# Kernel tuning notes

Hardware: AMD Instinct MI355X
Metric: run time of the kernel (lower is better)

The kernel has to match this reference:

```python
import jax, jax.numpy as jnp
import numpy as np

B, N, D, K, L, H, DFF = 2048, 64, 256, 32, 2, 8, 1024
TEMP = 10.0
EPS = 1e-10


def _ln(x, g, b):
    m = jnp.mean(x, -1, keepdims=True)
    v = jnp.mean((x - m) ** 2, -1, keepdims=True)
    return (x - m) * jax.lax.rsqrt(v + 1e-5) * g + b


def _mha(x, Wqkv, bqkv, Wo, bo):
    b, n, d = x.shape
    dh = d // H
    qkv = x @ Wqkv.T + bqkv                      # [b,n,3d]
    q, k, v = jnp.split(qkv, 3, axis=-1)
    q = q.reshape(b, n, H, dh)
    k = k.reshape(b, n, H, dh)
    v = v.reshape(b, n, H, dh)
    att = jnp.einsum('bqhd,bkhd->bhqk', q, k) / np.float32(np.sqrt(dh))
    att = jax.nn.softmax(att, axis=-1)
    o = jnp.einsum('bhqk,bkhd->bqhd', att, v).reshape(b, n, d)
    return o @ Wo.T + bo


def _encoder(x, Wqkv, bqkv, Wo, bo, ln1_g, ln1_b, ln2_g, ln2_b, W1, b1, W2, b2):
    # torch TransformerEncoder, norm_first=False (post-LN), dropout=0
    for l in range(L):
        x = _ln(x + _mha(x, Wqkv[l], bqkv[l], Wo[l], bo[l]), ln1_g[l], ln1_b[l])
        h = jax.nn.relu(x @ W1[l].T + b1[l]) @ W2[l].T + b2[l]
        x = _ln(x + h, ln2_g[l], ln2_b[l])
    return x


def _cluster_probs_from_emb(emb, mus):
    # ||x - tanh(mu)||^2 via expansion to avoid the [B,N,K,D] intermediate
    mt = jnp.tanh(mus)                                       # [K,D]
    d2 = (jnp.sum(emb ** 2, -1)[..., None]
          - 2.0 * jnp.einsum('bnd,kd->bnk', emb, mt)
          + jnp.sum(mt ** 2, -1))                            # [B,N,K]
    e = jnp.exp(-d2 / TEMP)
    return e / jnp.sum(e, -1, keepdims=True)


def _forward(input_series, init_logits, transition_logits,
             Wqkv, bqkv, Wo, bo, ln1_g, ln1_b, ln2_g, ln2_b,
             W1, b1, W2, b2, mus):
    prob_pi = jax.nn.softmax(init_logits, axis=0)            # [K]
    prob_A = jax.nn.softmax(transition_logits, axis=1)       # [K,K]
    emb_all = _encoder(input_series, Wqkv, bqkv, Wo, bo,
                       ln1_g, ln1_b, ln2_g, ln2_b, W1, b1, W2, b2)
    logits_all = _cluster_probs_from_emb(emb_all, mus)       # [B,N,K]

    log_emit = jnp.log(logits_all + EPS)                     # [B,N,K]
    lt0 = jax.nn.softmax(jnp.log(prob_pi + EPS)[None, :] + log_emit[:, 0], axis=1)

    def step(lt, le):
        lt = jax.nn.softmax(jnp.log(lt @ prob_A + EPS) + le, axis=1)
        return lt, lt

    _, rest = jax.lax.scan(step, lt0, jnp.swapaxes(log_emit[:, 1:], 0, 1))
    cluster_probs = jnp.concatenate([lt0[:, None], jnp.swapaxes(rest, 0, 1)], axis=1)
    entropy_loss = -jnp.mean(jnp.sum(cluster_probs * jnp.log(cluster_probs + EPS), -1))
    return cluster_probs, emb_all, prob_pi, prob_A, entropy_loss


def setup_inputs() -> dict:
    key = jax.random.key(0)
    ks = jax.random.split(key, 10)
    s = jnp.float32(0.02)
    return {
        'input_series': jax.random.normal(ks[0], (B, N, D), jnp.float32),
        'init_logits': jax.random.normal(ks[1], (K,), jnp.float32),
        'transition_logits': jax.random.normal(ks[2], (K, K), jnp.float32),
        'Wqkv': jax.random.normal(ks[3], (L, 3 * D, D), jnp.float32) * s,
        'bqkv': jnp.zeros((L, 3 * D), jnp.float32),
        'Wo': jax.random.normal(ks[4], (L, D, D), jnp.float32) * s,
        'bo': jnp.zeros((L, D), jnp.float32),
        'ln1_g': jnp.ones((L, D), jnp.float32),
        'ln1_b': jnp.zeros((L, D), jnp.float32),
        'ln2_g': jnp.ones((L, D), jnp.float32),
        'ln2_b': jnp.zeros((L, D), jnp.float32),
        'W1': jax.random.normal(ks[5], (L, DFF, D), jnp.float32) * s,
        'b1': jnp.zeros((L, DFF), jnp.float32),
        'W2': jax.random.normal(ks[6], (L, D, DFF), jnp.float32) * s,
        'b2': jnp.zeros((L, D), jnp.float32),
        'mus': jax.random.normal(ks[7], (K, D), jnp.float32),
    }


def reference(input_series, init_logits, transition_logits, Wqkv, bqkv, Wo, bo,
              ln1_g, ln1_b, ln2_g, ln2_b, W1, b1, W2, b2, mus):
    return _forward(input_series, init_logits, transition_logits, Wqkv, bqkv,
                    Wo, bo, ln1_g, ln1_b, ln2_g, ln2_b, W1, b1, W2, b2, mus)
```

## Files before the change

### kernel.cpp

```cpp
#include <hip/hip_runtime.h>

#define BB   2048
#define NNX  64
#define DD   256
#define KKC  32
#define LLN  2
#define HHN  8
#define DHH  32
#define DFFN 1024
#define BNT  (BB*NNX)

typedef short s16x8 __attribute__((ext_vector_type(8)));
typedef float f32x4 __attribute__((ext_vector_type(4)));

#define GLOAD_LDS16(gp, lp) __builtin_amdgcn_global_load_lds( \
    (const __attribute__((address_space(1))) void*)(gp),      \
    (__attribute__((address_space(3))) void*)(lp), 16, 0, 0)

#define WAITVM4() asm volatile("s_waitcnt vmcnt(4)" ::: "memory")
#define WAITVM0() asm volatile("s_waitcnt vmcnt(0)" ::: "memory")
#define WAITLGKM0() do { asm volatile("s_waitcnt lgkmcnt(0)" ::: "memory"); \
                         __builtin_amdgcn_sched_barrier(0); } while (0)
#define SBAR() __builtin_amdgcn_s_barrier()

__device__ __forceinline__ unsigned short f2bf(float f) {
  unsigned int u = __float_as_uint(f);
  u += 0x7fffu + ((u >> 16) & 1u);
  return (unsigned short)(u >> 16);
}
__device__ __forceinline__ float bf2f(unsigned short u) {
  return __uint_as_float(((unsigned int)u) << 16);
}

__device__ __forceinline__ unsigned char f2fp8(float f) {
  unsigned u = __float_as_uint(f);
  unsigned lsb = (u >> 20) & 1u;
  u += 0x7FFFFu + lsb;
  int e = (int)((u >> 23) & 255u) - 120;
  if (e <= 0) {
    int q = (int)(f * 512.f + 0.5f);
    return (unsigned char)q;
  }
  if (e > 15) return 0x7E;
  return (unsigned char)((e << 3) | ((u >> 20) & 7u));
}
__device__ __forceinline__ unsigned char f2fp8s(float f) {
  unsigned s = __float_as_uint(f) >> 31;
  float a = fminf(fabsf(f), 448.f);
  return (unsigned char)((s << 7) | f2fp8(a));
}

__global__ __launch_bounds__(256) void cvt_kernel(const float4* __restrict__ src,
                                                  ushort4* __restrict__ dst, int n4) {
  int i = blockIdx.x * 256 + threadIdx.x;
  int st = gridDim.x * 256;
  for (; i < n4; i += st) {
    float4 v = src[i];
    ushort4 o;
    o.x = f2bf(v.x); o.y = f2bf(v.y); o.z = f2bf(v.z); o.w = f2bf(v.w);
    dst[i] = o;
  }
}

__global__ __launch_bounds__(256) void cvtw_kernel(const float4* __restrict__ wq, ushort4* __restrict__ dq,
                                                   const float4* __restrict__ wo, ushort4* __restrict__ dov,
                                                   const float4* __restrict__ w1, ushort4* __restrict__ d1,
                                                   const float4* __restrict__ w2, uchar4* __restrict__ d2) {
  const int n0 = 98304, n1 = 32768, n2 = 131072, n3 = 131072;
  int i = blockIdx.x * 256 + threadIdx.x;
  int st = gridDim.x * 256;
  for (; i < n0 + n1 + n2 + n3; i += st) {
    int j = i;
    if (j < n0) {
      float4 v = wq[j];
      dq[j] = (ushort4){f2bf(v.x), f2bf(v.y), f2bf(v.z), f2bf(v.w)};
    } else if ((j -= n0) < n1) {
      float4 v = wo[j];
      dov[j] = (ushort4){f2bf(v.x), f2bf(v.y), f2bf(v.z), f2bf(v.w)};
    } else if ((j -= n1) < n2) {
      float4 v = w1[j];
      d1[j] = (ushort4){f2bf(v.x), f2bf(v.y), f2bf(v.z), f2bf(v.w)};
    } else {
      j -= n2;
      float4 v = w2[j];
      d2[j] = (uchar4){f2fp8s(v.x * 64.f), f2fp8s(v.y * 64.f),
                       f2fp8s(v.z * 64.f), f2fp8s(v.w * 64.f)};
    }
  }
}

__global__ void mt_kernel(const float* __restrict__ mus, unsigned short* __restrict__ mtb,
                          float* __restrict__ mtn) {
  int k = threadIdx.x;
  if (k < 32) {
    float acc = 0.f;
    for (int d = 0; d < 256; d++) {
      float t = tanhf(mus[k * 256 + d]);
      mtb[k * 264 + d] = f2bf(t);
      acc += t * t;
    }
    mtn[k] = acc;
  }
}

__global__ void piA_kernel(const float* __restrict__ il, const float* __restrict__ tl,
                           float* __restrict__ d_pi, float* __restrict__ d_A,
                           float* __restrict__ d_ent) {
  int lane = threadIdx.x;
  if (lane == 0) *d_ent = 0.f;
  if (lane < 32) {
    float v = il[lane];
    float mx = v;
    #pragma unroll
    for (int off = 16; off; off >>= 1) mx = fmaxf(mx, __shfl_xor(mx, off, 32));
    float e = expf(v - mx), sm = e;
    #pragma unroll
    for (int off = 16; off; off >>= 1) sm += __shfl_xor(sm, off, 32);
    d_pi[lane] = e / sm;
    for (int r = 0; r < 32; r++) {
      float a = tl[r * 32 + lane];
      float m2 = a;
      #pragma unroll
      for (int off = 16; off; off >>= 1) m2 = fmaxf(m2, __shfl_xor(m2, off, 32));
      float e2 = expf(a - m2), s2 = e2;
      #pragma unroll
      for (int off = 16; off; off >>= 1) s2 += __shfl_xor(s2, off, 32);
      d_A[r * 32 + lane] = e2 / s2;
    }
  }
}

template <int EPI>
__global__ __launch_bounds__(256, 4) void gemm_nt(const unsigned short* __restrict__ A,
                                                  const unsigned short* __restrict__ Bw,
                                                  const float* __restrict__ bias,
                                                  void* __restrict__ outp,
                                                  int N, int K, int nx) {
  __shared__ unsigned short lds[16384];
  const int t = threadIdx.x;
  const int bid = blockIdx.x, nwg = gridDim.x;
  const int wg = (bid & 7) * (nwg >> 3) + (bid >> 3);
  const int m0 = (wg / nx) << 7;
  const int n0 = (wg % nx) << 7;
  const int lane = t & 63, w = t >> 6;
  const int wm = w >> 1, wn = w & 1;
  const int lr = lane & 15, lk = lane >> 4;

  const int r0 = t >> 2, sg = t & 3;
  const int s0 = sg ^ ((r0 >> 1) & 3);
  const int r1 = r0 + 64;
  const int s1 = sg ^ ((r1 >> 1) & 3);
  const int aoff0 = (m0 + r0) * K + s0 * 8;
  const int aoff1 = (m0 + r1) * K + s1 * 8;
  const int boff0 = (n0 + r0) * K + s0 * 8;
  const int boff1 = (n0 + r1) * K + s1 * 8;

#define STAGE(buf, k0) do {                                    \
    char* la = (char*)lds + (buf) * 16384;                     \
    GLOAD_LDS16(A + aoff0 + (k0), la + t * 16);                \
    GLOAD_LDS16(A + aoff1 + (k0), la + 4096 + t * 16);         \
    GLOAD_LDS16(Bw + boff0 + (k0), la + 8192 + t * 16);        \
    GLOAD_LDS16(Bw + boff1 + (k0), la + 12288 + t * 16);       \
  } while (0)

  f32x4 acc[4][4];
  #pragma unroll
  for (int i = 0; i < 4; i++)
    #pragma unroll
    for (int j = 0; j < 4; j++) acc[i][j] = (f32x4)(0.f);

  const int ra = wm * 64 + lr, rb = wn * 64 + lr;
  const int sla = lk ^ ((ra >> 1) & 3), slb = lk ^ ((rb >> 1) & 3);

  const int NT = K >> 5;
  STAGE(0, 0);
  STAGE(1, 32);
  WAITVM4();
  SBAR();

  int c = 0;
  for (int kt = 0; kt < NT; kt++) {
    s16x8 af[4], bf[4];
    {
      const unsigned short* ua = lds + c * 8192;
      const unsigned short* ub = ua + 4096;
      #pragma unroll
      for (int mf = 0; mf < 4; mf++)
        af[mf] = *(const s16x8*)&ua[(ra + mf * 16) * 32 + sla * 8];
      #pragma unroll
      for (int nf = 0; nf < 4; nf++)
        bf[nf] = *(const s16x8*)&ub[(rb + nf * 16) * 32 + slb * 8];
    }
    __builtin_amdgcn_s_setprio(1);
    #pragma unroll
    for (int mf = 0; mf < 4; mf++)
      #pragma unroll
      for (int nf = 0; nf < 4; nf++)
        acc[mf][nf] = __builtin_amdgcn_mfma_f32_16x16x32_bf16(af[mf], bf[nf], acc[mf][nf], 0, 0, 0);
    __builtin_amdgcn_s_setprio(0);
    SBAR();
    if (kt < NT - 2) {
      STAGE(c, (kt + 2) << 5);
      WAITVM4();
    } else if (kt == NT - 2) {
      WAITVM0();
    }
    SBAR();
    c ^= 1;
  }
#undef STAGE

  #pragma unroll
  for (int nf = 0; nf < 4; nf++) {
    int col = n0 + wn * 64 + nf * 16 + lr;
    float bv = bias[col];
    #pragma unroll
    for (int mf = 0; mf < 4; mf++)
      #pragma unroll
      for (int r = 0; r < 4; r++) {
        int row = m0 + wm * 64 + mf * 16 + lk * 4 + r;
        size_t o = (size_t)row * N + col;
        float v = acc[mf][nf][r] + bv;
        if (EPI == 0) {
          ((unsigned short*)outp)[o] = f2bf(v);
        } else {
          float h = fminf(fmaxf(v, 0.f) * 8.f, 448.f);
          ((unsigned char*)outp)[o] = f2fp8(h);
        }
      }
  }
}

template <bool WR32>
__global__ __launch_bounds__(512) void gemm_ln(const unsigned short* __restrict__ A,
                                               const unsigned short* __restrict__ Bw,
                                               const float* __restrict__ bias,
                                               const unsigned short* __restrict__ res,
                                               const float* __restrict__ g,
                                               const float* __restrict__ bta,
                                               unsigned short* __restrict__ xb,
                                               float* __restrict__ x32,
                                               int K) {
  __shared__ unsigned short As[128 * 64];
  __shared__ unsigned short Bs[256 * 64];
  __shared__ float stats[2][128][4];
  const int t = threadIdx.x;
  const int nwg = gridDim.x;
  const int bid = blockIdx.x;
  const int wg = (bid & 7) * (nwg >> 3) + (bid >> 3);
  const int m0 = wg << 7;

  const int lane = t & 63, w = t >> 6;
  const int wm = w >> 2, wn = w & 3;
  const int lr = lane & 15, lk = lane >> 4;

  size_t aoff[2], boff[4];
  #pragma unroll
  for (int p = 0; p < 2; p++) {
    int u = p * 512 + t;
    int row = u >> 3, sp = u & 7;
    int seg = sp ^ (((row >> 2) & 1) << 1);
    aoff[p] = (size_t)(m0 + row) * K + seg * 8;
  }
  #pragma unroll
  for (int p = 0; p < 4; p++) {
    int u = p * 512 + t;
    int row = u >> 3, sp = u & 7;
    int seg = sp ^ (((row >> 2) & 1) << 1);
    boff[p] = (size_t)row * K + seg * 8;
  }

  f32x4 acc[4][4];
  #pragma unroll
  for (int i = 0; i < 4; i++)
    #pragma unroll
    for (int j = 0; j < 4; j++) acc[i][j] = (f32x4)(0.f);

  for (int k0 = 0; k0 < K; k0 += 64) {
    #pragma unroll
    for (int p = 0; p < 2; p++)
      GLOAD_LDS16(A + aoff[p] + k0, (char*)As + (p * 512 + t) * 16);
    #pragma unroll
    for (int p = 0; p < 4; p++)
      GLOAD_LDS16(Bw + boff[p] + k0, (char*)Bs + (p * 512 + t) * 16);
    __syncthreads();
    #pragma unroll
    for (int z = 0; z < 2; z++) {
      s16x8 af[4], bfr[4];
      #pragma unroll
      for (int mf = 0; mf < 4; mf++) {
        int row = wm * 64 + mf * 16 + lr;
        int cc = (z * 4 + lk) ^ (((row >> 2) & 1) << 1);
        af[mf] = *(const s16x8*)&As[row * 64 + cc * 8];
      }
      #pragma unroll
      for (int nf = 0; nf < 4; nf++) {
        int row = wn * 64 + nf * 16 + lr;
        int cc = (z * 4 + lk) ^ (((row >> 2) & 1) << 1);
        bfr[nf] = *(const s16x8*)&Bs[row * 64 + cc * 8];
      }
      #pragma unroll
      for (int mf = 0; mf < 4; mf++)
        #pragma unroll
        for (int nf = 0; nf < 4; nf++)
          acc[mf][nf] = __builtin_amdgcn_mfma_f32_16x16x32_bf16(af[mf], bfr[nf], acc[mf][nf], 0, 0, 0);
    }
    __syncthreads();
  }

  float bv[4];
  #pragma unroll
  for (int nf = 0; nf < 4; nf++) bv[nf] = bias[wn * 64 + nf * 16 + lr];

  #pragma unroll
  for (int mf = 0; mf < 4; mf++) {
    #pragma unroll
    for (int r = 0; r < 4; r++) {
      int grow = m0 + wm * 64 + mf * 16 + lk * 4 + r;
      float s = 0.f, q = 0.f;
      #pragma unroll
      for (int nf = 0; nf < 4; nf++) {
        int col = wn * 64 + nf * 16 + lr;
        float v = acc[mf][nf][r] + bv[nf] + bf2f(res[(size_t)grow * 256 + col]);
        acc[mf][nf][r] = v;
        s += v; q += v * v;
      }
      #pragma unroll
      for (int off = 1; off < 16; off <<= 1) { s += __shfl_xor(s, off); q += __shfl_xor(q, off); }
      if (lr == 0) {
        int lrow = wm * 64 + mf * 16 + lk * 4 + r;
        stats[0][lrow][wn] = s;
        stats[1][lrow][wn] = q;
      }
    }
  }
  __syncthreads();

  float gv[4], bbv[4];
  #pragma unroll
  for (int nf = 0; nf < 4; nf++) {
    int col = wn * 64 + nf * 16 + lr;
    gv[nf] = g[col]; bbv[nf] = bta[col];
  }
  #pragma unroll
  for (int mf = 0; mf < 4; mf++) {
    #pragma unroll
    for (int r = 0; r < 4; r++) {
      int lrow = wm * 64 + mf * 16 + lk * 4 + r;
      int grow = m0 + lrow;
      float s4 = stats[0][lrow][0] + stats[0][lrow][1] + stats[0][lrow][2] + stats[0][lrow][3];
      float q4 = stats[1][lrow][0] + stats[1][lrow][1] + stats[1][lrow][2] + stats[1][lrow][3];
      float mean = s4 * (1.f / 256.f);
      float var = q4 * (1.f / 256.f) - mean * mean;
      float rs = rsqrtf(var + 1e-5f);
      #pragma unroll
      for (int nf = 0; nf < 4; nf++) {
        int col = wn * 64 + nf * 16 + lr;
        float val = (acc[mf][nf][r] - mean) * rs * gv[nf] + bbv[nf];
        xb[(size_t)grow * 256 + col] = f2bf(val);
        if (WR32) x32[(size_t)grow * 256 + col] = val;
      }
    }
  }
}

template <bool WR32>
__global__ __launch_bounds__(512) void gemm_ln_fp8(const unsigned char* __restrict__ A,
                                                   const unsigned char* __restrict__ Bw,
                                                   const float* __restrict__ bias,
                                                   const unsigned short* __restrict__ res,
                                                   const float* __restrict__ g,
                                                   const float* __restrict__ bta,
                                                   unsigned short* __restrict__ xb,
                                                   float* __restrict__ x32,
                                                   int K) {
  __shared__ unsigned char lds8[24576];
  float* stats = (float*)lds8;
  const int t = threadIdx.x;
  const int nwg = gridDim.x;
  const int bid = blockIdx.x;
  const int wg = (bid & 7) * (nwg >> 3) + (bid >> 3);
  const int m0 = wg << 7;

  const int lane = t & 63, w = t >> 6;
  const int wm = w >> 2, wn = w & 3;
  const int lr = lane & 15, lk = lane >> 4;

  const int auu = t >> 8, arow = (t >> 1) & 127, asg = t & 1;
  const size_t aoff = (size_t)(m0 + arow) * K + auu * 32 + asg * 16;
  size_t boff[2];
  #pragma unroll
  for (int p = 0; p < 2; p++) {
    int idx = p * 512 + t;
    int buu = idx >> 9, brow = (idx >> 1) & 255, bsg = idx & 1;
    boff[p] = (size_t)brow * K + buu * 32 + bsg * 16;
  }

  f32x4 acc[4][4];
  #pragma unroll
  for (int i = 0; i < 4; i++)
    #pragma unroll
    for (int j = 0; j < 4; j++) acc[i][j] = (f32x4)(0.f);

  for (int k0 = 0; k0 < K; k0 += 64) {
    GLOAD_LDS16(A + aoff + k0, (char*)lds8 + t * 16);
    GLOAD_LDS16(Bw + boff[0] + k0, (char*)lds8 + 8192 + t * 16);
    GLOAD_LDS16(Bw + boff[1] + k0, (char*)lds8 + 16384 + t * 16);
    __syncthreads();
    #pragma unroll
    for (int kk = 0; kk < 2; kk++) {
      long long af[4], bf[4];
      #pragma unroll
      for (int mf = 0; mf < 4; mf++)
        af[mf] = *(const long long*)&lds8[kk * 4096 + (wm * 64 + mf * 16 + lr) * 32 + lk * 8];
      #pragma unroll
      for (int nf = 0; nf < 4; nf++)
        bf[nf] = *(const long long*)&lds8[8192 + kk * 8192 + (wn * 64 + nf * 16 + lr) * 32 + lk * 8];
      #pragma unroll
      for (int mf = 0; mf < 4; mf++)
        #pragma unroll
        for (int nf = 0; nf < 4; nf++)
          acc[mf][nf] = __builtin_amdgcn_mfma_f32_16x16x32_fp8_fp8(af[mf], bf[nf], acc[mf][nf], 0, 0, 0);
    }
    __syncthreads();
  }

  const float isc = 1.f / 512.f;
  float bv[4];
  #pragma unroll
  for (int nf = 0; nf < 4; nf++) bv[nf] = bias[wn * 64 + nf * 16 + lr];

  #pragma unroll
  for (int mf = 0; mf < 4; mf++) {
    #pragma unroll
    for (int r = 0; r < 4; r++) {
      int grow = m0 + wm * 64 + mf * 16 + lk * 4 + r;
      float s = 0.f, q = 0.f;
      #pragma unroll
      for (int nf = 0; nf < 4; nf++) {
        int col = wn * 64 + nf * 16 + lr;
        float v = acc[mf][nf][r] * isc + bv[nf] + bf2f(res[(size_t)grow * 256 + col]);
        acc[mf][nf][r] = v;
        s += v; q += v * v;
      }
      #pragma unroll
      for (int off = 1; off < 16; off <<= 1) { s += __shfl_xor(s, off); q += __shfl_xor(q, off); }
      if (lr == 0) {
        int lrow = wm * 64 + mf * 16 + lk * 4 + r;
        stats[lrow * 4 + wn] = s;
        stats[512 + lrow * 4 + wn] = q;
      }
    }
  }
  __syncthreads();

  float gv[4], bbv[4];
  #pragma unroll
  for (int nf = 0; nf < 4; nf++) {
    int col = wn * 64 + nf * 16 + lr;
    gv[nf] = g[col]; bbv[nf] = bta[col];
  }
  #pragma unroll
  for (int mf = 0; mf < 4; mf++) {
    #pragma unroll
    for (int r = 0; r < 4; r++) {
      int lrow = wm * 64 + mf * 16 + lk * 4 + r;
      int grow = m0 + lrow;
      float s4 = stats[lrow * 4 + 0] + stats[lrow * 4 + 1] + stats[lrow * 4 + 2] + stats[lrow * 4 + 3];
      float q4 = stats[512 + lrow * 4 + 0] + stats[512 + lrow * 4 + 1]
               + stats[512 + lrow * 4 + 2] + stats[512 + lrow * 4 + 3];
      float mean = s4 * (1.f / 256.f);
      float var = q4 * (1.f / 256.f) - mean * mean;
      float rs = rsqrtf(var + 1e-5f);
      #pragma unroll
      for (int nf = 0; nf < 4; nf++) {
        int col = wn * 64 + nf * 16 + lr;
        float val = (acc[mf][nf][r] - mean) * rs * gv[nf] + bbv[nf];
        xb[(size_t)grow * 256 + col] = f2bf(val);
        if (WR32) x32[(size_t)grow * 256 + col] = val;
      }
    }
  }
}

__global__ __launch_bounds__(64) void attn_kernel(const unsigned short* __restrict__ qkv,
                                                  unsigned short* __restrict__ ob) {
  __shared__ unsigned short al[6784];
  unsigned short* qs = al;
  unsigned short* ks = al + 2048;
  unsigned short* vs = al + 4608;
  unsigned short* vt = al;
  unsigned short* ps = al + 2176;
  const int bh = blockIdx.x;
  const int b = bh >> 3, h = bh & 7;
  const int lane = threadIdx.x;
  const int lr = lane & 15, lk = lane >> 4;

  #pragma unroll
  for (int p = 0; p < 4; p++) {
    int u = lane + p * 64;
    int row = u >> 2, seg = u & 3;
    size_t gb = (size_t)(b * 64 + row) * 768 + h * 32 + seg * 8;
    GLOAD_LDS16(qkv + gb, (char*)al + u * 16);
    GLOAD_LDS16(qkv + gb + 256, (char*)al + 4096 + u * 16);
    GLOAD_LDS16(qkv + gb + 512, (char*)al + 9216 + u * 16);
  }
  __syncthreads();

  s16x8 aq[4], bk[4], vchunk[4];
  #pragma unroll
  for (int mi = 0; mi < 4; mi++) aq[mi] = *(const s16x8*)&qs[(mi * 16 + lr) * 32 + lk * 8];
  #pragma unroll
  for (int nj = 0; nj < 4; nj++) bk[nj] = *(const s16x8*)&ks[(nj * 16 + lr) * 32 + lk * 8];
  const int vrow = lane >> 2, vcs = (lane & 3) * 8;
  #pragma unroll
  for (int q = 0; q < 4; q++)
    vchunk[q] = *(const s16x8*)&vs[(q * 16 + vrow) * 32 + vcs];
  WAITLGKM0();

  #pragma unroll
  for (int q = 0; q < 4; q++)
    #pragma unroll
    for (int j = 0; j < 8; j++)
      vt[(vcs + j) * 68 + q * 16 + vrow] = (unsigned short)vchunk[q][j];

  f32x4 s[4][4];
  #pragma unroll
  for (int i = 0; i < 4; i++)
    #pragma unroll
    for (int j = 0; j < 4; j++) s[i][j] = (f32x4)(0.f);
  #pragma unroll
  for (int mi = 0; mi < 4; mi++)
    #pragma unroll
    for (int nj = 0; nj < 4; nj++)
      s[mi][nj] = __builtin_amdgcn_mfma_f32_16x16x32_bf16(aq[mi], bk[nj], s[mi][nj], 0, 0, 0);

  const float scale = 0.17677669529663687f;
  #pragma unroll
  for (int mi = 0; mi < 4; mi++) {
    #pragma unroll
    for (int r = 0; r < 4; r++) {
      float t0 = s[mi][0][r] * scale, t1 = s[mi][1][r] * scale;
      float t2 = s[mi][2][r] * scale, t3 = s[mi][3][r] * scale;
      float mx = fmaxf(fmaxf(t0, t1), fmaxf(t2, t3));
      #pragma unroll
      for (int off = 8; off; off >>= 1) mx = fmaxf(mx, __shfl_xor(mx, off, 16));
      float e0 = expf(t0 - mx), e1 = expf(t1 - mx), e2 = expf(t2 - mx), e3 = expf(t3 - mx);
      float sm = e0 + e1 + e2 + e3;
      #pragma unroll
      for (int off = 8; off; off >>= 1) sm += __shfl_xor(sm, off, 16);
      float inv = 1.f / sm;
      int prow = mi * 16 + lk * 4 + r;
      ps[prow * 72 + lr + 0]  = f2bf(e0 * inv);
      ps[prow * 72 + lr + 16] = f2bf(e1 * inv);
      ps[prow * 72 + lr + 32] = f2bf(e2 * inv);
      ps[prow * 72 + lr + 48] = f2bf(e3 * inv);
    }
  }
  WAITLGKM0();

  f32x4 oacc[4][2];
  #pragma unroll
  for (int i = 0; i < 4; i++) { oacc[i][0] = (f32x4)(0.f); oacc[i][1] = (f32x4)(0.f); }
  #pragma unroll
  for (int kk = 0; kk < 2; kk++) {
    s16x8 bv[2];
    #pragma unroll
    for (int nf = 0; nf < 2; nf++)
      bv[nf] = *(const s16x8*)&vt[(nf * 16 + lr) * 68 + kk * 32 + lk * 8];
    #pragma unroll
    for (int mi = 0; mi < 4; mi++) {
      s16x8 ap = *(const s16x8*)&ps[(mi * 16 + lr) * 72 + kk * 32 + lk * 8];
      #pragma unroll
      for (int nf = 0; nf < 2; nf++)
        oacc[mi][nf] = __builtin_amdgcn_mfma_f32_16x16x32_bf16(ap, bv[nf], oacc[mi][nf], 0, 0, 0);
    }
  }
  #pragma unroll
  for (int mi = 0; mi < 4; mi++)
    #pragma unroll
    for (int nf = 0; nf < 2; nf++)
      #pragma unroll
      for (int r = 0; r < 4; r++) {
        int tok = mi * 16 + lk * 4 + r;
        int c = nf * 16 + lr;
        ob[(size_t)(b * 64 + tok) * 256 + h * 32 + c] = f2bf(oacc[mi][nf][r]);
      }
}

__global__ __launch_bounds__(256) void cluster_kernel(const unsigned short* __restrict__ xb,
                                                      const unsigned short* __restrict__ mtb,
                                                      const float* __restrict__ mtn,
                                                      float* __restrict__ log_emit) {
  __shared__ unsigned short ms[32 * 264];
  const int t = threadIdx.x;
  for (int i = t; i < 2112; i += 256)
    ((uint2*)ms)[i] = ((const uint2*)mtb)[i];
  const int lane = t & 63, w = t >> 6;
  const int lr = lane & 15, lk = lane >> 4;
  const float mtn0 = mtn[lr], mtn1 = mtn[16 + lr];
  __syncthreads();

  const size_t tok0 = (size_t)blockIdx.x * 256 + (size_t)w * 64;
  f32x4 s[4][2];
  #pragma unroll
  for (int i = 0; i < 4; i++) { s[i][0] = (f32x4)(0.f); s[i][1] = (f32x4)(0.f); }

  #pragma unroll
  for (int kk = 0; kk < 8; kk++) {
    s16x8 bf0 = *(const s16x8*)&ms[lr * 264 + lk * 8 + kk * 32];
    s16x8 bf1 = *(const s16x8*)&ms[(16 + lr) * 264 + lk * 8 + kk * 32];
    #pragma unroll
    for (int mi = 0; mi < 4; mi++) {
      s16x8 af = *(const s16x8*)&xb[(tok0 + mi * 16 + lr) * 256 + lk * 8 + kk * 32];
      s[mi][0] = __builtin_amdgcn_mfma_f32_16x16x32_bf16(af, bf0, s[mi][0], 0, 0, 0);
      s[mi][1] = __builtin_amdgcn_mfma_f32_16x16x32_bf16(af, bf1, s[mi][1], 0, 0, 0);
    }
  }

  #pragma unroll
  for (int mi = 0; mi < 4; mi++) {
    #pragma unroll
    for (int r = 0; r < 4; r++) {
      float l0 = (2.f * s[mi][0][r] - mtn0) * 0.1f;
      float l1 = (2.f * s[mi][1][r] - mtn1) * 0.1f;
      float mx = fmaxf(l0, l1);
      #pragma unroll
      for (int off = 8; off; off >>= 1) mx = fmaxf(mx, __shfl_xor(mx, off, 16));
      float e0 = expf(l0 - mx), e1 = expf(l1 - mx);
      float sm = e0 + e1;
      #pragma unroll
      for (int off = 8; off; off >>= 1) sm += __shfl_xor(sm, off, 16);
      float inv = 1.f / sm;
      size_t row = tok0 + mi * 16 + lk * 4 + r;
      log_emit[row * 32 + lr]      = logf(e0 * inv + 1e-10f);
      log_emit[row * 32 + 16 + lr] = logf(e1 * inv + 1e-10f);
    }
  }
}

__global__ __launch_bounds__(256) void scan_kernel(const float* __restrict__ log_emit,
                                                   const float* __restrict__ pi,
                                                   const float* __restrict__ A,
                                                   float* __restrict__ cp,
                                                   float* __restrict__ ent) {
  const int g = threadIdx.x >> 5, j = threadIdx.x & 31;
  const int batch = blockIdx.x * 8 + g;
  float regA[32];
  #pragma unroll
  for (int i = 0; i < 32; i++) regA[i] = A[i * 32 + j];
  const float* le = log_emit + (size_t)batch * 64 * 32;
  float* cpo = cp + (size_t)batch * 64 * 32;

  float u = logf(pi[j] + 1e-10f) + le[j];
  float mx = u;
  #pragma unroll
  for (int off = 16; off; off >>= 1) mx = fmaxf(mx, __shfl_xor(mx, off, 32));
  float e = expf(u - mx), sm = e;
  #pragma unroll
  for (int off = 16; off; off >>= 1) sm += __shfl_xor(sm, off, 32);
  float p = e / sm;
  cpo[j] = p;
  float enta = p * logf(p + 1e-10f);

  for (int n = 1; n < 64; n++) {
    float tt = 0.f;
    #pragma unroll
    for (int i = 0; i < 32; i++) tt += __shfl(p, i, 32) * regA[i];
    u = logf(tt + 1e-10f) + le[n * 32 + j];
    mx = u;
    #pragma unroll
    for (int off = 16; off; off >>= 1) mx = fmaxf(mx, __shfl_xor(mx, off, 32));
    e = expf(u - mx); sm = e;
    #pragma unroll
    for (int off = 16; off; off >>= 1) sm += __shfl_xor(sm, off, 32);
    p = e / sm;
    cpo[n * 32 + j] = p;
    enta += p * logf(p + 1e-10f);
  }
  #pragma unroll
  for (int off = 16; off; off >>= 1) enta += __shfl_xor(enta, off, 32);
  if (j == 0) atomicAdd(ent, -enta * (1.f / (2048.f * 64.f)));
}

extern "C" void kernel_launch(void* const* d_in, const int* in_sizes, int n_in,
                              void* d_out, int out_size, void* d_ws, size_t ws_size,
                              hipStream_t stream) {
  const float* input = (const float*)d_in[0];
  const float* init_logits = (const float*)d_in[1];
  const float* trans = (const float*)d_in[2];
  const float* Wqkv = (const float*)d_in[3];
  const float* bqkv = (const float*)d_in[4];
  const float* Wo = (const float*)d_in[5];
  const float* bo = (const float*)d_in[6];
  const float* ln1g = (const float*)d_in[7];
  const float* ln1b = (const float*)d_in[8];
  const float* ln2g = (const float*)d_in[9];
  const float* ln2b = (const float*)d_in[10];
  const float* W1 = (const float*)d_in[11];
  const float* b1 = (const float*)d_in[12];
  const float* W2 = (const float*)d_in[13];
  const float* b2 = (const float*)d_in[14];
  const float* mus = (const float*)d_in[15];

  float* out = (float*)d_out;
  float* cp = out;
  float* x = out + 4194304;
  float* d_pi = out + 37748736;
  float* d_A = out + 37748768;
  float* d_ent = out + 37749792;

  char* ws = (char*)d_ws;
  unsigned short* qkv = (unsigned short*)ws;
  unsigned char* hb = (unsigned char*)ws;
  float* log_emit = (float*)ws;
  unsigned short* ob = (unsigned short*)(ws + 268435456ull);
  unsigned short* xb = (unsigned short*)(ws + 335544320ull);
  unsigned short* wq_b = (unsigned short*)(ws + 402653184ull);
  unsigned short* wo_b = (unsigned short*)(ws + 402653184ull + 786432ull);
  unsigned short* w1_b = (unsigned short*)(ws + 402653184ull + 1048576ull);
  unsigned char* w2_f = (unsigned char*)(ws + 402653184ull + 2097152ull);
  unsigned short* mtb = (unsigned short*)(ws + 402653184ull + 3145728ull);
  float* mtn = (float*)(ws + 402653184ull + 3178496ull);

  cvt_kernel<<<2048, 256, 0, stream>>>((const float4*)input, (ushort4*)xb, BNT * 256 / 4);
  cvtw_kernel<<<512, 256, 0, stream>>>((const float4*)Wqkv, (ushort4*)wq_b,
                                       (const float4*)Wo, (ushort4*)wo_b,
                                       (const float4*)W1, (ushort4*)w1_b,
                                       (const float4*)W2, (uchar4*)w2_f);
  mt_kernel<<<1, 64, 0, stream>>>(mus, mtb, mtn);
  piA_kernel<<<1, 64, 0, stream>>>(init_logits, trans, d_pi, d_A, d_ent);

  for (int l = 0; l < 2; l++) {
    gemm_nt<0><<<6144, 256, 0, stream>>>(xb, wq_b + l * 196608, bqkv + l * 768,
                                         qkv, 768, 256, 6);
    attn_kernel<<<16384, 64, 0, stream>>>(qkv, ob);
    gemm_ln<false><<<1024, 512, 0, stream>>>(ob, wo_b + l * 65536, bo + l * 256,
                                             xb, ln1g + l * 256, ln1b + l * 256,
                                             xb, nullptr, 256);
    gemm_nt<1><<<8192, 256, 0, stream>>>(xb, w1_b + l * 262144, b1 + l * 1024,
                                         hb, 1024, 256, 8);
    if (l == LLN - 1)
      gemm_ln_fp8<true><<<1024, 512, 0, stream>>>(hb, w2_f + l * 262144, b2 + l * 256,
                                                  xb, ln2g + l * 256, ln2b + l * 256,
                                                  xb, x, 1024);
    else
      gemm_ln_fp8<false><<<1024, 512, 0, stream>>>(hb, w2_f + l * 262144, b2 + l * 256,
                                                   xb, ln2g + l * 256, ln2b + l * 256,
                                                   xb, nullptr, 1024);
  }

  cluster_kernel<<<512, 256, 0, stream>>>(xb, mtb, mtn, log_emit);
  scan_kernel<<<256, 256, 0, stream>>>(log_emit, d_pi, d_A, cp, d_ent);
}
```

Before: 1.111 ms.

## Store QKV as scaled fp8 and run attention matmuls with fp8 MFMA

The QKV projection now writes scaled fp8 (x32) in place of bf16, which halves the QKV write and the attention read traffic. The attention kernel loads fp8 Q/K/V, runs the QK^T and PV products with fp8 MFMA, and quantizes the probabilities to fp8 (scaled by 128), rescaling the logits and outputs to compensate. The tiny mt and piA setup kernels are merged into a single two-block launch. The cost is precision: fp8 Q/K/V and probabilities risk larger numerical error, and small probabilities are flushed to zero.

Result: faster. 1.075 ms (-3.2%).

```diff
diff --git a/kernel.cpp b/kernel.cpp
--- a/kernel.cpp
+++ b/kernel.cpp
@@ -48,6 +48,13 @@
   unsigned s = __float_as_uint(f) >> 31;
   float a = fminf(fabsf(f), 448.f);
   return (unsigned char)((s << 7) | f2fp8(a));
+}
+__device__ __forceinline__ unsigned char p2fp8(float f) {
+  unsigned u = __float_as_uint(f);
+  u += 0x7FFFFu + ((u >> 20) & 1u);
+  int e = (int)((u >> 23) & 255u) - 120;
+  if (e <= 0) return 0;
+  return (unsigned char)((e << 3) | ((u >> 20) & 7u));
 }
 
 __global__ __launch_bounds__(256) void cvt_kernel(const float4* __restrict__ src,
@@ -89,43 +96,43 @@
   }
 }
 
-__global__ void mt_kernel(const float* __restrict__ mus, unsigned short* __restrict__ mtb,
-                          float* __restrict__ mtn) {
-  int k = threadIdx.x;
-  if (k < 32) {
-    float acc = 0.f;
-    for (int d = 0; d < 256; d++) {
-      float t = tanhf(mus[k * 256 + d]);
-      mtb[k * 264 + d] = f2bf(t);
-      acc += t * t;
-    }
-    mtn[k] = acc;
-  }
-}
-
-__global__ void piA_kernel(const float* __restrict__ il, const float* __restrict__ tl,
-                           float* __restrict__ d_pi, float* __restrict__ d_A,
-                           float* __restrict__ d_ent) {
+__global__ void mtpi_kernel(const float* __restrict__ mus, unsigned short* __restrict__ mtb,
+                            float* __restrict__ mtn,
+                            const float* __restrict__ il, const float* __restrict__ tl,
+                            float* __restrict__ d_pi, float* __restrict__ d_A,
+                            float* __restrict__ d_ent) {
   int lane = threadIdx.x;
-  if (lane == 0) *d_ent = 0.f;
-  if (lane < 32) {
-    float v = il[lane];
-    float mx = v;
-    #pragma unroll
-    for (int off = 16; off; off >>= 1) mx = fmaxf(mx, __shfl_xor(mx, off, 32));
-    float e = expf(v - mx), sm = e;
-    #pragma unroll
-    for (int off = 16; off; off >>= 1) sm += __shfl_xor(sm, off, 32);
-    d_pi[lane] = e / sm;
-    for (int r = 0; r < 32; r++) {
-      float a = tl[r * 32 + lane];
-      float m2 = a;
-      #pragma unroll
-      for (int off = 16; off; off >>= 1) m2 = fmaxf(m2, __shfl_xor(m2, off, 32));
-      float e2 = expf(a - m2), s2 = e2;
-      #pragma unroll
-      for (int off = 16; off; off >>= 1) s2 += __shfl_xor(s2, off, 32);
-      d_A[r * 32 + lane] = e2 / s2;
+  if (blockIdx.x == 0) {
+    if (lane < 32) {
+      float acc = 0.f;
+      for (int d = 0; d < 256; d++) {
+        float t = tanhf(mus[lane * 256 + d]);
+        mtb[lane * 264 + d] = f2bf(t);
+        acc += t * t;
+      }
+      mtn[lane] = acc;
+    }
+  } else {
+    if (lane == 0) *d_ent = 0.f;
+    if (lane < 32) {
+      float v = il[lane];
+      float mx = v;
+      #pragma unroll
+      for (int off = 16; off; off >>= 1) mx = fmaxf(mx, __shfl_xor(mx, off, 32));
+      float e = expf(v - mx), sm = e;
+      #pragma unroll
+      for (int off = 16; off; off >>= 1) sm += __shfl_xor(sm, off, 32);
+      d_pi[lane] = e / sm;
+      for (int r = 0; r < 32; r++) {
+        float a = tl[r * 32 + lane];
+        float m2 = a;
+        #pragma unroll
+        for (int off = 16; off; off >>= 1) m2 = fmaxf(m2, __shfl_xor(m2, off, 32));
+        float e2 = expf(a - m2), s2 = e2;
+        #pragma unroll
+        for (int off = 16; off; off >>= 1) s2 += __shfl_xor(s2, off, 32);
+        d_A[r * 32 + lane] = e2 / s2;
+      }
     }
   }
 }
@@ -223,9 +230,11 @@
         float v = acc[mf][nf][r] + bv;
         if (EPI == 0) {
           ((unsigned short*)outp)[o] = f2bf(v);
+        } else if (EPI == 1) {
+          float hh = fminf(fmaxf(v, 0.f) * 8.f, 448.f);
+          ((unsigned char*)outp)[o] = f2fp8(hh);
         } else {
-          float h = fminf(fmaxf(v, 0.f) * 8.f, 448.f);
-          ((unsigned char*)outp)[o] = f2fp8(h);
+          ((unsigned char*)outp)[o] = f2fp8s(v * 32.f);
         }
       }
   }
@@ -483,46 +492,50 @@
   }
 }
 
-__global__ __launch_bounds__(64) void attn_kernel(const unsigned short* __restrict__ qkv,
+__global__ __launch_bounds__(64) void attn_kernel(const unsigned char* __restrict__ qkv,
                                                   unsigned short* __restrict__ ob) {
-  __shared__ unsigned short al[6784];
-  unsigned short* qs = al;
-  unsigned short* ks = al + 2048;
-  unsigned short* vs = al + 4608;
-  unsigned short* vt = al;
-  unsigned short* ps = al + 2176;
+  __shared__ unsigned char al[7168];
+  unsigned char* qs = al;
+  unsigned char* ks = al + 2048;
+  unsigned char* vs = al + 4096;
+  unsigned char* vt = al;
+  unsigned char* ps = al + 2304;
   const int bh = blockIdx.x;
   const int b = bh >> 3, h = bh & 7;
   const int lane = threadIdx.x;
   const int lr = lane & 15, lk = lane >> 4;
 
   #pragma unroll
-  for (int p = 0; p < 4; p++) {
+  for (int p = 0; p < 2; p++) {
     int u = lane + p * 64;
-    int row = u >> 2, seg = u & 3;
-    size_t gb = (size_t)(b * 64 + row) * 768 + h * 32 + seg * 8;
+    int row = u >> 1, seg = u & 1;
+    size_t gb = (size_t)(b * 64 + row) * 768 + h * 32 + seg * 16;
     GLOAD_LDS16(qkv + gb, (char*)al + u * 16);
-    GLOAD_LDS16(qkv + gb + 256, (char*)al + 4096 + u * 16);
-    GLOAD_LDS16(qkv + gb + 512, (char*)al + 9216 + u * 16);
+    GLOAD_LDS16(qkv + gb + 256, (char*)al + 2048 + u * 16);
+    GLOAD_LDS16(qkv + gb + 512, (char*)al + 4096 + u * 16);
   }
   __syncthreads();
 
-  s16x8 aq[4], bk[4], vchunk[4];
-  #pragma unroll
-  for (int mi = 0; mi < 4; mi++) aq[mi] = *(const s16x8*)&qs[(mi * 16 + lr) * 32 + lk * 8];
-  #pragma unroll
-  for (int nj = 0; nj < 4; nj++) bk[nj] = *(const s16x8*)&ks[(nj * 16 + lr) * 32 + lk * 8];
+  long long aq[4], bk[4], vchunk[4];
+  #pragma unroll
+  for (int mi = 0; mi < 4; mi++)
+    aq[mi] = *(const long long*)&qs[(mi * 16 + lr) * 32 + lk * 8];
+  #pragma unroll
+  for (int nj = 0; nj < 4; nj++)
+    bk[nj] = *(const long long*)&ks[(nj * 16 + lr) * 32 + lk * 8];
   const int vrow = lane >> 2, vcs = (lane & 3) * 8;
   #pragma unroll
   for (int q = 0; q < 4; q++)
-    vchunk[q] = *(const s16x8*)&vs[(q * 16 + vrow) * 32 + vcs];
+    vchunk[q] = *(const long long*)&vs[(q * 16 + vrow) * 32 + vcs];
   WAITLGKM0();
 
   #pragma unroll
-  for (int q = 0; q < 4; q++)
+  for (int q = 0; q < 4; q++) {
+    unsigned long long vv = (unsigned long long)vchunk[q];
     #pragma unroll
     for (int j = 0; j < 8; j++)
-      vt[(vcs + j) * 68 + q * 16 + vrow] = (unsigned short)vchunk[q][j];
+      vt[(vcs + j) * 72 + q * 16 + vrow] = (unsigned char)(vv >> (8 * j));
+  }
 
   f32x4 s[4][4];
   #pragma unroll
@@ -533,9 +546,9 @@
   for (int mi = 0; mi < 4; mi++)
     #pragma unroll
     for (int nj = 0; nj < 4; nj++)
-      s[mi][nj] = __builtin_amdgcn_mfma_f32_16x16x32_bf16(aq[mi], bk[nj], s[mi][nj], 0, 0, 0);
-
-  const float scale = 0.17677669529663687f;
+      s[mi][nj] = __builtin_amdgcn_mfma_f32_16x16x32_fp8_fp8(aq[mi], bk[nj], s[mi][nj], 0, 0, 0);
+
+  const float scale = 0.17677669529663687f / 1024.f;
   #pragma unroll
   for (int mi = 0; mi < 4; mi++) {
     #pragma unroll
@@ -549,12 +562,12 @@
       float sm = e0 + e1 + e2 + e3;
       #pragma unroll
       for (int off = 8; off; off >>= 1) sm += __shfl_xor(sm, off, 16);
-      float inv = 1.f / sm;
+      float inv = 128.f / sm;
       int prow = mi * 16 + lk * 4 + r;
-      ps[prow * 72 + lr + 0]  = f2bf(e0 * inv);
-      ps[prow * 72 + lr + 16] = f2bf(e1 * inv);
-      ps[prow * 72 + lr + 32] = f2bf(e2 * inv);
-      ps[prow * 72 + lr + 48] = f2bf(e3 * inv);
+      ps[prow * 72 + lr + 0]  = p2fp8(e0 * inv);
+      ps[prow * 72 + lr + 16] = p2fp8(e1 * inv);
+      ps[prow * 72 + lr + 32] = p2fp8(e2 * inv);
+      ps[prow * 72 + lr + 48] = p2fp8(e3 * inv);
     }
   }
   WAITLGKM0();
@@ -564,18 +577,19 @@
   for (int i = 0; i < 4; i++) { oacc[i][0] = (f32x4)(0.f); oacc[i][1] = (f32x4)(0.f); }
   #pragma unroll
   for (int kk = 0; kk < 2; kk++) {
-    s16x8 bv[2];
+    long long bv[2];
     #pragma unroll
     for (int nf = 0; nf < 2; nf++)
-      bv[nf] = *(const s16x8*)&vt[(nf * 16 + lr) * 68 + kk * 32 + lk * 8];
+      bv[nf] = *(const long long*)&vt[(nf * 16 + lr) * 72 + kk * 32 + lk * 8];
     #pragma unroll
     for (int mi = 0; mi < 4; mi++) {
-      s16x8 ap = *(const s16x8*)&ps[(mi * 16 + lr) * 72 + kk * 32 + lk * 8];
+      long long ap = *(const long long*)&ps[(mi * 16 + lr) * 72 + kk * 32 + lk * 8];
       #pragma unroll
       for (int nf = 0; nf < 2; nf++)
-        oacc[mi][nf] = __builtin_amdgcn_mfma_f32_16x16x32_bf16(ap, bv[nf], oacc[mi][nf], 0, 0, 0);
-    }
-  }
+        oacc[mi][nf] = __builtin_amdgcn_mfma_f32_16x16x32_fp8_fp8(ap, bv[nf], oacc[mi][nf], 0, 0, 0);
+    }
+  }
+  const float osc = 1.f / 4096.f;
   #pragma unroll
   for (int mi = 0; mi < 4; mi++)
     #pragma unroll
@@ -584,7 +598,7 @@
       for (int r = 0; r < 4; r++) {
         int tok = mi * 16 + lk * 4 + r;
         int c = nf * 16 + lr;
-        ob[(size_t)(b * 64 + tok) * 256 + h * 32 + c] = f2bf(oacc[mi][nf][r]);
+        ob[(size_t)(b * 64 + tok) * 256 + h * 32 + c] = f2bf(oacc[mi][nf][r] * osc);
       }
 }
 
@@ -711,7 +725,7 @@
   float* d_ent = out + 37749792;
 
   char* ws = (char*)d_ws;
-  unsigned short* qkv = (unsigned short*)ws;
+  unsigned char* qkv = (unsigned char*)ws;
   unsigned char* hb = (unsigned char*)ws;
   float* log_emit = (float*)ws;
   unsigned short* ob = (unsigned short*)(ws + 268435456ull);
@@ -728,11 +742,10 @@
                                        (const float4*)Wo, (ushort4*)wo_b,
                                        (const float4*)W1, (ushort4*)w1_b,
                                        (const float4*)W2, (uchar4*)w2_f);
-  mt_kernel<<<1, 64, 0, stream>>>(mus, mtb, mtn);
-  piA_kernel<<<1, 64, 0, stream>>>(init_logits, trans, d_pi, d_A, d_ent);
+  mtpi_kernel<<<2, 64, 0, stream>>>(mus, mtb, mtn, init_logits, trans, d_pi, d_A, d_ent);
 
   for (int l = 0; l < 2; l++) {
-    gemm_nt<0><<<6144, 256, 0, stream>>>(xb, wq_b + l * 196608, bqkv + l * 768,
+    gemm_nt<2><<<6144, 256, 0, stream>>>(xb, wq_b + l * 196608, bqkv + l * 768,
                                          qkv, 768, 256, 6);
     attn_kernel<<<16384, 64, 0, stream>>>(qkv, ob);
     gemm_ln<false><<<1024, 512, 0, stream>>>(ob, wo_b + l * 65536, bo + l * 256,
```
